# Kernel optimization log

Hardware: AMD Instinct MI355X
Metric: run time of the kernel (lower is better)

The kernel has to match this reference:

```python
import jax, jax.numpy as jnp
import numpy as np

B, S, D, H = 4, 2048, 1024, 16
DH = D // H  # per-head depth = 64


def setup_inputs() -> dict:
    key = jax.random.key(0)
    kq, kk, kv = jax.random.split(key, 3)
    q = jax.random.normal(kq, (B, S, D), dtype=jnp.float32)
    k = jax.random.normal(kk, (B, S, D), dtype=jnp.float32)
    v = jax.random.normal(kv, (B, S, D), dtype=jnp.float32)
    # Standard look-ahead mask: 1.0 where attention is disallowed (j > i).
    mask = (1.0 - jnp.tril(jnp.ones((S, S), dtype=jnp.float32)))[None, None, :, :]
    return {"q": q, "k": k, "v": v, "mask": mask, "training": 0}


def _split_heads(x):
    # [B, S, D] -> [B, H, S, DH]
    b, s, _ = x.shape
    return x.reshape(b, s, H, DH).transpose(0, 2, 1, 3)


def reference(q, k, v, mask, training):
    qh, kh, vh = _split_heads(q), _split_heads(k), _split_heads(v)
    scale = 1.0 / jnp.sqrt(jnp.float32(DH))
    logits = jnp.einsum("bhqd,bhkd->bhqk", qh, kh) * scale  # [B,H,S,S]
    logits = logits + mask * (-1e9)
    weights = jax.nn.softmax(logits, axis=-1)
    attn = jnp.einsum("bhqk,bhkd->bhqd", weights, vh)  # [B,H,S,DH]
    out = attn.transpose(0, 2, 1, 3).reshape(q.shape[0], 1, -1, H * DH)  # [B,1,S,D]
    return out
```

## Files before the change

### kernel.cpp

```cpp
#include <hip/hip_runtime.h>
#include <hip/hip_bf16.h>


constexpr int Ss = 2048, Dd = 1024, Hh = 16, DH = 64, Bb = 4;
constexpr float QSCALE = 0.125f * 1.44269504088896f;
constexpr float MFIX2 = 13.0f;
constexpr float MFIXF = 9.0f;

typedef _Float16 half2_t __attribute__((ext_vector_type(2)));
typedef _Float16 half4_t __attribute__((ext_vector_type(4)));
typedef _Float16 half8_t __attribute__((ext_vector_type(8)));
typedef __attribute__((ext_vector_type(4))) float floatx4;
typedef __attribute__((ext_vector_type(8))) short short8;

union H8 { half8_t v; half2_t h2[4]; };

__device__ __forceinline__ half2_t pk(float a, float b) {
  return __builtin_bit_cast(half2_t, __builtin_amdgcn_cvt_pkrtz(a, b));
}
__device__ __forceinline__ float fexp2(float x) {
#if __has_builtin(__builtin_amdgcn_exp2f)
  return __builtin_amdgcn_exp2f(x);
#else
  return __exp2f(x);
#endif
}
__device__ __forceinline__ unsigned short f2bf(float f) {
  union { float f; unsigned u; } x; x.f = f;
  unsigned r = x.u + 0x7FFFu + ((x.u >> 16) & 1u);
  return (unsigned short)(r >> 16);
}
__device__ __forceinline__ unsigned short f2bf_trunc(float f) {
  union { float f; unsigned u; } x; x.f = f;
  return (unsigned short)(x.u >> 16);
}
__device__ __forceinline__ void async_cp16(const unsigned short* g, unsigned short* l) {
  __builtin_amdgcn_global_load_lds(
      (const __attribute__((address_space(1))) unsigned int*)g,
      (__attribute__((address_space(3))) unsigned int*)l, 16, 0, 0);
}

__global__ __launch_bounds__(256)
void prep_kv(const float* __restrict__ Kg, const float* __restrict__ Vg,
             unsigned short* __restrict__ Kh, unsigned short* __restrict__ Vt) {
  __shared__ float tile[64][65];
  const int s0 = (int)blockIdx.x * 64;
  const int bh = (int)blockIdx.y;
  const int b = bh >> 4, h = bh & 15;
  const int t = threadIdx.x;
  const int sl = t >> 2, qtr = t & 3;

  const size_t inoff = ((size_t)(b * Ss + s0 + sl)) * Dd + h * DH + qtr * 16;
  const float* krow = Kg + inoff;
  const float* vrow = Vg + inoff;
  const int pout = (2 * (sl >> 5) + ((sl & 7) >> 2)) * 16 + ((sl >> 3) & 3) * 4 + (sl & 3);
  unsigned short* kout = Kh + ((size_t)bh * Ss + s0 + pout) * 64 + qtr * 16;

  #pragma unroll
  for (int i = 0; i < 2; ++i) {
    float4 k0 = ((const float4*)krow)[i * 2 + 0];
    float4 k1 = ((const float4*)krow)[i * 2 + 1];
    H8 o;
    o.h2[0] = pk(k0.x, k0.y); o.h2[1] = pk(k0.z, k0.w);
    o.h2[2] = pk(k1.x, k1.y); o.h2[3] = pk(k1.z, k1.w);
    *(half8_t*)(kout + i * 8) = o.v;
  }
  #pragma unroll
  for (int i = 0; i < 4; ++i) {
    float4 v = ((const float4*)vrow)[i];
    tile[sl][qtr * 16 + i * 4 + 0] = v.x;
    tile[sl][qtr * 16 + i * 4 + 1] = v.y;
    tile[sl][qtr * 16 + i * 4 + 2] = v.z;
    tile[sl][qtr * 16 + i * 4 + 3] = v.w;
  }
  __syncthreads();
  const int d = t >> 2, kc = t & 3;
  unsigned short* orow = Vt + ((size_t)bh * DH + d) * Ss + s0 + kc * 16;
  #pragma unroll
  for (int i = 0; i < 2; ++i) {
    H8 o;
    o.h2[0] = pk(tile[kc * 16 + i * 8 + 0][d], tile[kc * 16 + i * 8 + 1][d]);
    o.h2[1] = pk(tile[kc * 16 + i * 8 + 2][d], tile[kc * 16 + i * 8 + 3][d]);
    o.h2[2] = pk(tile[kc * 16 + i * 8 + 4][d], tile[kc * 16 + i * 8 + 5][d]);
    o.h2[3] = pk(tile[kc * 16 + i * 8 + 6][d], tile[kc * 16 + i * 8 + 7][d]);
    *(half8_t*)(orow + i * 8) = o.v;
  }
}

__global__ __launch_bounds__(256, 2)
void mha_fa9(const float* __restrict__ Qg, const unsigned short* __restrict__ Kh,
             const unsigned short* __restrict__ Vt, float* __restrict__ Og) {
  __shared__ __align__(16) unsigned short Kld[2][128 * 64];
  __shared__ __align__(16) unsigned short Vld[2][64 * 128];

  const int tid = threadIdx.x;
  const int wave = tid >> 6, lane = tid & 63;
  const int c = lane & 15, qd = lane >> 4;
  const int bh = (int)blockIdx.x;
  const int b = bh >> 4, h = bh & 15;
  const int slot = (int)blockIdx.y;
  const int t = (slot < 4) ? slot : 11 - slot;
  const int Qt[2] = {2 * t + 1, 2 * t};
  const int nkt = 2 * t + 2;

  const unsigned short* kbase = Kh + (size_t)bh * Ss * 64;
  const unsigned short* vbase = Vt + (size_t)bh * DH * Ss;
  float* obase = Og + (size_t)b * Ss * Dd + h * DH;

  auto stage = [&](int kt, int bufi) {
    const unsigned short* ktile = kbase + kt * 128 * 64;
    #pragma unroll
    for (int it = 0; it < 4; ++it) {
      int p = (it * 4 + wave) * 64 + lane;
      int r = p >> 3, pos = p & 7, j = pos ^ (r & 7);
      async_cp16(ktile + r * 64 + j * 8, &Kld[bufi][(it * 4 + wave) * 512]);
    }
    #pragma unroll
    for (int it = 0; it < 4; ++it) {
      int p = (it * 4 + wave) * 64 + lane;
      int d = p >> 4, c16 = p & 15;
      int j = (c16 & 8) | ((c16 ^ d) & 7);
      async_cp16(vbase + (size_t)d * Ss + kt * 128 + j * 8,
                 &Vld[bufi][(it * 4 + wave) * 512]);
    }
  };

  auto load_frags = [&](const unsigned short* Kl, const unsigned short* Vl, int kb,
                        half8_t (&kf0)[4], half8_t (&kf1)[4], half8_t (&w8)[4][2]) {
    #pragma unroll
    for (int f = 0; f < 4; ++f) {
      int kk = kb * 64 + f * 16 + c;
      kf0[f] = *(const half8_t*)&Kl[kk * 64 + (qd ^ (c & 7)) * 8];
      kf1[f] = *(const half8_t*)&Kl[kk * 64 + ((4 + qd) ^ (c & 7)) * 8];
    }
    #pragma unroll
    for (int f = 0; f < 4; ++f) {
      int rr = f * 16 + c;
      #pragma unroll
      for (int wnd = 0; wnd < 2; ++wnd) {
        int chi = kb * 8 + wnd * 4 + qd;
        int phys = (chi & 8) | ((chi ^ rr) & 7);
        w8[f][wnd] = *(const half8_t*)&Vl[rr * 128 + phys * 8];
      }
    }
  };

  const half8_t ones8 = {(_Float16)1.f, (_Float16)1.f, (_Float16)1.f, (_Float16)1.f,
                         (_Float16)1.f, (_Float16)1.f, (_Float16)1.f, (_Float16)1.f};

  half8_t qf[2][2][2];
  #pragma unroll
  for (int ti = 0; ti < 2; ++ti) {
    #pragma unroll
    for (int mi = 0; mi < 2; ++mi) {
      const float* qr =
          Qg + ((size_t)b * Ss + Qt[ti] * 128 + mi * 64 + wave * 16 + c) * Dd + h * DH;
      #pragma unroll
      for (int ks = 0; ks < 2; ++ks) {
        float4 a0 = ((const float4*)(qr + ks * 32 + qd * 8))[0];
        float4 a1 = ((const float4*)(qr + ks * 32 + qd * 8))[1];
        H8 f;
        f.h2[0] = pk(a0.x * QSCALE, a0.y * QSCALE);
        f.h2[1] = pk(a0.z * QSCALE, a0.w * QSCALE);
        f.h2[2] = pk(a1.x * QSCALE, a1.y * QSCALE);
        f.h2[3] = pk(a1.z * QSCALE, a1.w * QSCALE);
        qf[ti][mi][ks] = f.v;
      }
    }
  }

  floatx4 o_acc[2][2][4];
  floatx4 l_acc[2][2];
  #pragma unroll
  for (int ti = 0; ti < 2; ++ti)
    #pragma unroll
    for (int mi = 0; mi < 2; ++mi) {
      #pragma unroll
      for (int f = 0; f < 4; ++f) o_acc[ti][mi][f] = (floatx4){0.f, 0.f, 0.f, 0.f};
      l_acc[ti][mi] = (floatx4){0.f, 0.f, 0.f, 0.f};
    }

  auto compute_kb = [&](int kb0g, const half8_t (&kf0)[4], const half8_t (&kf1)[4],
                        const half8_t (&w8)[4][2]) {
    #pragma unroll
    for (int ti = 0; ti < 2; ++ti) {
      #pragma unroll
      for (int mi = 0; mi < 2; ++mi) {
        const int qlo = Qt[ti] * 128 + mi * 64 + wave * 16;
        if (kb0g > qlo + 15) continue;

        floatx4 s[4];
        #pragma unroll
        for (int f = 0; f < 4; ++f) s[f] = (floatx4){0.f, 0.f, 0.f, 0.f};
        __builtin_amdgcn_s_setprio(1);
        #pragma unroll
        for (int f = 0; f < 4; ++f) {
          s[f] = __builtin_amdgcn_mfma_f32_16x16x32_f16(kf0[f], qf[ti][mi][0], s[f], 0, 0, 0);
          s[f] = __builtin_amdgcn_mfma_f32_16x16x32_f16(kf1[f], qf[ti][mi][1], s[f], 0, 0, 0);
        }
        __builtin_amdgcn_s_setprio(0);
        if (kb0g + 63 > qlo) {
          #pragma unroll
          for (int f = 0; f < 4; ++f) {
            int keyb = kb0g + ((f >> 1) << 5) + ((f & 1) << 2) + qd * 8;
            #pragma unroll
            for (int r = 0; r < 4; ++r)
              if (keyb + r > qlo + c) s[f][r] = -1e30f;
          }
        }
        half8_t p8[2];
        #pragma unroll
        for (int wnd = 0; wnd < 2; ++wnd) {
          H8 pp;
          pp.h2[0] = pk(fexp2(s[2 * wnd][0] - MFIX2), fexp2(s[2 * wnd][1] - MFIX2));
          pp.h2[1] = pk(fexp2(s[2 * wnd][2] - MFIX2), fexp2(s[2 * wnd][3] - MFIX2));
          pp.h2[2] = pk(fexp2(s[2 * wnd + 1][0] - MFIX2), fexp2(s[2 * wnd + 1][1] - MFIX2));
          pp.h2[3] = pk(fexp2(s[2 * wnd + 1][2] - MFIX2), fexp2(s[2 * wnd + 1][3] - MFIX2));
          p8[wnd] = pp.v;
        }
        __builtin_amdgcn_s_setprio(1);
        #pragma unroll
        for (int fd = 0; fd < 4; ++fd) {
          #pragma unroll
          for (int wnd = 0; wnd < 2; ++wnd)
            o_acc[ti][mi][fd] = __builtin_amdgcn_mfma_f32_16x16x32_f16(
                p8[wnd], w8[fd][wnd], o_acc[ti][mi][fd], 0, 0, 0);
        }
        #pragma unroll
        for (int wnd = 0; wnd < 2; ++wnd)
          l_acc[ti][mi] = __builtin_amdgcn_mfma_f32_16x16x32_f16(p8[wnd], ones8,
                                                                 l_acc[ti][mi], 0, 0, 0);
        __builtin_amdgcn_s_setprio(0);
      }
    }
  };

  asm volatile("s_waitcnt vmcnt(0)" ::: "memory");
  stage(0, 0);
  stage(1, 1);

  for (int kt = 0; kt < nkt; ++kt) {
    const int bufi = kt & 1;
    if (kt + 1 < nkt) {
      asm volatile("s_waitcnt vmcnt(8)" ::: "memory");
    } else {
      asm volatile("s_waitcnt vmcnt(0)" ::: "memory");
    }
    __builtin_amdgcn_s_barrier();

    const unsigned short* Kl = Kld[bufi];
    const unsigned short* Vl = Vld[bufi];

    half8_t kf0a[4], kf1a[4], w8a[4][2];
    load_frags(Kl, Vl, 0, kf0a, kf1a, w8a);
    compute_kb(kt * 128, kf0a, kf1a, w8a);

    half8_t kf0b[4], kf1b[4], w8b[4][2];
    load_frags(Kl, Vl, 1, kf0b, kf1b, w8b);
    asm volatile("s_waitcnt lgkmcnt(0)" ::: "memory");
    __builtin_amdgcn_s_barrier();
    if (kt + 2 < nkt) stage(kt + 2, bufi);

    compute_kb(kt * 128 + 64, kf0b, kf1b, w8b);
  }

  #pragma unroll
  for (int ti = 0; ti < 2; ++ti)
    #pragma unroll
    for (int mi = 0; mi < 2; ++mi)
      #pragma unroll
      for (int r = 0; r < 4; ++r) {
        float inv = 1.f / l_acc[ti][mi][r];
        size_t row = (size_t)(Qt[ti] * 128 + mi * 64 + wave * 16 + qd * 4 + r);
        #pragma unroll
        for (int f = 0; f < 4; ++f)
          obase[row * Dd + f * 16 + c] = o_acc[ti][mi][f][r] * inv;
      }
}

__global__ __launch_bounds__(256, 4)
void mha_fwd(const float* __restrict__ Qg, const float* __restrict__ Kg,
             const float* __restrict__ Vg, float* __restrict__ Og) {
  __shared__ __align__(16) unsigned short Kldf[64 * 72];
  __shared__ __align__(16) unsigned short Vtldf[64 * 72];
  __shared__ __align__(16) unsigned short Pldf[4 * 16 * 72];
  const int tid = threadIdx.x, wave = tid >> 6, lane = tid & 63;
  const int c = lane & 15, qd = lane >> 4;
  const int qt = (Ss / 64 - 1) - (int)blockIdx.x;
  const int b = (int)blockIdx.y >> 4, h = (int)blockIdx.y & 15;
  const float* qbase = Qg + (size_t)b * Ss * Dd + h * DH;
  const float* kbase = Kg + (size_t)b * Ss * Dd + h * DH;
  const float* vbase = Vg + (size_t)b * Ss * Dd + h * DH;
  short8 qfrag[2];
  {
    const float* qr = qbase + (size_t)(qt * 64 + wave * 16 + c) * Dd + qd * 8;
    for (int ks = 0; ks < 2; ++ks) {
      float4 a0 = ((const float4*)(qr + ks * 32))[0];
      float4 a1 = ((const float4*)(qr + ks * 32))[1];
      short8 f;
      f[0] = (short)f2bf(a0.x * 0.125f); f[1] = (short)f2bf(a0.y * 0.125f);
      f[2] = (short)f2bf(a0.z * 0.125f); f[3] = (short)f2bf(a0.w * 0.125f);
      f[4] = (short)f2bf(a1.x * 0.125f); f[5] = (short)f2bf(a1.y * 0.125f);
      f[6] = (short)f2bf(a1.z * 0.125f); f[7] = (short)f2bf(a1.w * 0.125f);
      qfrag[ks] = f;
    }
  }
  floatx4 o_acc[4];
  for (int f = 0; f < 4; ++f) o_acc[f] = (floatx4){0.f, 0.f, 0.f, 0.f};
  float l_lane[4] = {0.f, 0.f, 0.f, 0.f};
  const int row_g = qt * 64 + wave * 16;
  const int pbase = wave * 16 * 72;
  for (int kt = 0; kt <= qt; ++kt) {
    __syncthreads();
    {
      const int r = tid >> 2, quarter = tid & 3;
      const float* krow = kbase + (size_t)(kt * 64 + r) * Dd + quarter * 16;
      const float* vrow = vbase + (size_t)(kt * 64 + r) * Dd + quarter * 16;
      for (int i = 0; i < 4; ++i) {
        float4 kv = ((const float4*)krow)[i];
        int col = quarter * 16 + i * 4;
        ushort4 kk;
        kk.x = f2bf(kv.x); kk.y = f2bf(kv.y); kk.z = f2bf(kv.z); kk.w = f2bf(kv.w);
        *(ushort4*)&Kldf[r * 72 + col] = kk;
        float4 vv = ((const float4*)vrow)[i];
        Vtldf[(col + 0) * 72 + r] = f2bf(vv.x);
        Vtldf[(col + 1) * 72 + r] = f2bf(vv.y);
        Vtldf[(col + 2) * 72 + r] = f2bf(vv.z);
        Vtldf[(col + 3) * 72 + r] = f2bf(vv.w);
      }
    }
    __syncthreads();
    floatx4 s_acc[4];
    for (int f = 0; f < 4; ++f) s_acc[f] = (floatx4){0.f, 0.f, 0.f, 0.f};
    for (int f = 0; f < 4; ++f)
      for (int ks = 0; ks < 2; ++ks) {
        short8 kf = *(const short8*)&Kldf[(f * 16 + c) * 72 + ks * 32 + qd * 8];
        s_acc[f] = __builtin_amdgcn_mfma_f32_16x16x32_bf16(qfrag[ks], kf, s_acc[f], 0, 0, 0);
      }
    if (kt == qt)
      for (int f = 0; f < 4; ++f) {
        int key = kt * 64 + f * 16 + c;
        for (int r = 0; r < 4; ++r)
          if (key > row_g + qd * 4 + r) s_acc[f][r] = -1e30f;
      }
    for (int f = 0; f < 4; ++f)
      for (int r = 0; r < 4; ++r) {
        float p = __expf(s_acc[f][r] - MFIXF);
        l_lane[r] += p;
        Pldf[pbase + (qd * 4 + r) * 72 + f * 16 + c] = f2bf_trunc(p);
      }
    short8 pfrag[2];
    pfrag[0] = *(const short8*)&Pldf[pbase + c * 72 + qd * 8];
    pfrag[1] = *(const short8*)&Pldf[pbase + c * 72 + 32 + qd * 8];
    for (int f = 0; f < 4; ++f)
      for (int ks = 0; ks < 2; ++ks) {
        short8 vf = *(const short8*)&Vtldf[(f * 16 + c) * 72 + ks * 32 + qd * 8];
        o_acc[f] = __builtin_amdgcn_mfma_f32_16x16x32_bf16(pfrag[ks], vf, o_acc[f], 0, 0, 0);
      }
  }
  float* obase = Og + (size_t)b * Ss * Dd + h * DH;
  for (int r = 0; r < 4; ++r) {
    float lv = l_lane[r];
    lv += __shfl_xor(lv, 1); lv += __shfl_xor(lv, 2);
    lv += __shfl_xor(lv, 4); lv += __shfl_xor(lv, 8);
    float inv_l = 1.f / lv;
    size_t rowoff = (size_t)(row_g + qd * 4 + r) * Dd;
    for (int f = 0; f < 4; ++f)
      obase[rowoff + f * 16 + c] = o_acc[f][r] * inv_l;
  }
}

extern "C" void kernel_launch(void* const* d_in, const int* in_sizes, int n_in,
                              void* d_out, int out_size, void* d_ws, size_t ws_size,
                              hipStream_t stream) {
  const float* q = (const float*)d_in[0];
  const float* k = (const float*)d_in[1];
  const float* v = (const float*)d_in[2];
  float* out = (float*)d_out;

  const size_t elems = (size_t)Bb * Hh * Ss * DH;
  if (ws_size >= 2 * elems * 2) {
    unsigned short* kh = (unsigned short*)d_ws;
    unsigned short* vt = kh + elems;
    prep_kv<<<dim3(Ss / 64, Bb * Hh), 256, 0, stream>>>(k, v, kh, vt);
    mha_fa9<<<dim3(Bb * Hh, 8), 256, 0, stream>>>(q, kh, vt, out);
  } else {
    mha_fwd<<<dim3(Ss / 64, Bb * Hh), 256, 0, stream>>>(q, k, v, out);
  }
}
```

Baseline: 201.9 us.

## Split attention block across 8 waves, one 64-row half per wave group

The fused attention kernel now launches 512 threads per block instead of 256. The mi (64-row half) loop becomes a wave index, so each wave handles half the query rows and keeps half the accumulators and Q fragments. K/V staging is spread over 8 waves with fewer copies each, and the vmcnt wait threshold is adjusted to match. The aim is more waves in flight to hide latency and a lower per-wave register footprint, at the cost of every wave reading the full K/V fragments from LDS (more LDS traffic per FLOP) and a heavier barrier.

```diff
diff --git a/kernel.cpp b/kernel.cpp
--- a/kernel.cpp
+++ b/kernel.cpp
@@ -87,14 +87,15 @@
   }
 }
 
-__global__ __launch_bounds__(256, 2)
-void mha_fa9(const float* __restrict__ Qg, const unsigned short* __restrict__ Kh,
-             const unsigned short* __restrict__ Vt, float* __restrict__ Og) {
+__global__ __launch_bounds__(512, 4)
+void mha_fa10(const float* __restrict__ Qg, const unsigned short* __restrict__ Kh,
+              const unsigned short* __restrict__ Vt, float* __restrict__ Og) {
   __shared__ __align__(16) unsigned short Kld[2][128 * 64];
   __shared__ __align__(16) unsigned short Vld[2][64 * 128];
 
   const int tid = threadIdx.x;
   const int wave = tid >> 6, lane = tid & 63;
+  const int wv = wave & 3, mi = wave >> 2;
   const int c = lane & 15, qd = lane >> 4;
   const int bh = (int)blockIdx.x;
   const int b = bh >> 4, h = bh & 15;
@@ -110,18 +111,20 @@
   auto stage = [&](int kt, int bufi) {
     const unsigned short* ktile = kbase + kt * 128 * 64;
     #pragma unroll
-    for (int it = 0; it < 4; ++it) {
-      int p = (it * 4 + wave) * 64 + lane;
+    for (int it = 0; it < 2; ++it) {
+      int idx = it * 8 + wave;
+      int p = idx * 64 + lane;
       int r = p >> 3, pos = p & 7, j = pos ^ (r & 7);
-      async_cp16(ktile + r * 64 + j * 8, &Kld[bufi][(it * 4 + wave) * 512]);
-    }
-    #pragma unroll
-    for (int it = 0; it < 4; ++it) {
-      int p = (it * 4 + wave) * 64 + lane;
+      async_cp16(ktile + r * 64 + j * 8, &Kld[bufi][idx * 512]);
+    }
+    #pragma unroll
+    for (int it = 0; it < 2; ++it) {
+      int idx = it * 8 + wave;
+      int p = idx * 64 + lane;
       int d = p >> 4, c16 = p & 15;
       int j = (c16 & 8) | ((c16 ^ d) & 7);
       async_cp16(vbase + (size_t)d * Ss + kt * 128 + j * 8,
-                 &Vld[bufi][(it * 4 + wave) * 512]);
+                 &Vld[bufi][idx * 512]);
     }
   };
 
@@ -148,90 +151,82 @@
   const half8_t ones8 = {(_Float16)1.f, (_Float16)1.f, (_Float16)1.f, (_Float16)1.f,
                          (_Float16)1.f, (_Float16)1.f, (_Float16)1.f, (_Float16)1.f};
 
-  half8_t qf[2][2][2];
+  half8_t qf[2][2];
   #pragma unroll
   for (int ti = 0; ti < 2; ++ti) {
-    #pragma unroll
-    for (int mi = 0; mi < 2; ++mi) {
-      const float* qr =
-          Qg + ((size_t)b * Ss + Qt[ti] * 128 + mi * 64 + wave * 16 + c) * Dd + h * DH;
-      #pragma unroll
-      for (int ks = 0; ks < 2; ++ks) {
-        float4 a0 = ((const float4*)(qr + ks * 32 + qd * 8))[0];
-        float4 a1 = ((const float4*)(qr + ks * 32 + qd * 8))[1];
-        H8 f;
-        f.h2[0] = pk(a0.x * QSCALE, a0.y * QSCALE);
-        f.h2[1] = pk(a0.z * QSCALE, a0.w * QSCALE);
-        f.h2[2] = pk(a1.x * QSCALE, a1.y * QSCALE);
-        f.h2[3] = pk(a1.z * QSCALE, a1.w * QSCALE);
-        qf[ti][mi][ks] = f.v;
-      }
-    }
-  }
-
-  floatx4 o_acc[2][2][4];
-  floatx4 l_acc[2][2];
-  #pragma unroll
-  for (int ti = 0; ti < 2; ++ti)
-    #pragma unroll
-    for (int mi = 0; mi < 2; ++mi) {
-      #pragma unroll
-      for (int f = 0; f < 4; ++f) o_acc[ti][mi][f] = (floatx4){0.f, 0.f, 0.f, 0.f};
-      l_acc[ti][mi] = (floatx4){0.f, 0.f, 0.f, 0.f};
-    }
+    const float* qr =
+        Qg + ((size_t)b * Ss + Qt[ti] * 128 + mi * 64 + wv * 16 + c) * Dd + h * DH;
+    #pragma unroll
+    for (int ks = 0; ks < 2; ++ks) {
+      float4 a0 = ((const float4*)(qr + ks * 32 + qd * 8))[0];
+      float4 a1 = ((const float4*)(qr + ks * 32 + qd * 8))[1];
+      H8 f;
+      f.h2[0] = pk(a0.x * QSCALE, a0.y * QSCALE);
+      f.h2[1] = pk(a0.z * QSCALE, a0.w * QSCALE);
+      f.h2[2] = pk(a1.x * QSCALE, a1.y * QSCALE);
+      f.h2[3] = pk(a1.z * QSCALE, a1.w * QSCALE);
+      qf[ti][ks] = f.v;
+    }
+  }
+
+  floatx4 o_acc[2][4];
+  floatx4 l_acc[2];
+  #pragma unroll
+  for (int ti = 0; ti < 2; ++ti) {
+    #pragma unroll
+    for (int f = 0; f < 4; ++f) o_acc[ti][f] = (floatx4){0.f, 0.f, 0.f, 0.f};
+    l_acc[ti] = (floatx4){0.f, 0.f, 0.f, 0.f};
+  }
 
   auto compute_kb = [&](int kb0g, const half8_t (&kf0)[4], const half8_t (&kf1)[4],
                         const half8_t (&w8)[4][2]) {
     #pragma unroll
     for (int ti = 0; ti < 2; ++ti) {
-      #pragma unroll
-      for (int mi = 0; mi < 2; ++mi) {
-        const int qlo = Qt[ti] * 128 + mi * 64 + wave * 16;
-        if (kb0g > qlo + 15) continue;
-
-        floatx4 s[4];
-        #pragma unroll
-        for (int f = 0; f < 4; ++f) s[f] = (floatx4){0.f, 0.f, 0.f, 0.f};
-        __builtin_amdgcn_s_setprio(1);
+      const int qlo = Qt[ti] * 128 + mi * 64 + wv * 16;
+      if (kb0g > qlo + 15) continue;
+
+      floatx4 s[4];
+      #pragma unroll
+      for (int f = 0; f < 4; ++f) s[f] = (floatx4){0.f, 0.f, 0.f, 0.f};
+      __builtin_amdgcn_s_setprio(1);
+      #pragma unroll
+      for (int f = 0; f < 4; ++f) {
+        s[f] = __builtin_amdgcn_mfma_f32_16x16x32_f16(kf0[f], qf[ti][0], s[f], 0, 0, 0);
+        s[f] = __builtin_amdgcn_mfma_f32_16x16x32_f16(kf1[f], qf[ti][1], s[f], 0, 0, 0);
+      }
+      __builtin_amdgcn_s_setprio(0);
+      if (kb0g + 63 > qlo) {
         #pragma unroll
         for (int f = 0; f < 4; ++f) {
-          s[f] = __builtin_amdgcn_mfma_f32_16x16x32_f16(kf0[f], qf[ti][mi][0], s[f], 0, 0, 0);
-          s[f] = __builtin_amdgcn_mfma_f32_16x16x32_f16(kf1[f], qf[ti][mi][1], s[f], 0, 0, 0);
+          int keyb = kb0g + ((f >> 1) << 5) + ((f & 1) << 2) + qd * 8;
+          #pragma unroll
+          for (int r = 0; r < 4; ++r)
+            if (keyb + r > qlo + c) s[f][r] = -1e30f;
         }
-        __builtin_amdgcn_s_setprio(0);
-        if (kb0g + 63 > qlo) {
-          #pragma unroll
-          for (int f = 0; f < 4; ++f) {
-            int keyb = kb0g + ((f >> 1) << 5) + ((f & 1) << 2) + qd * 8;
-            #pragma unroll
-            for (int r = 0; r < 4; ++r)
-              if (keyb + r > qlo + c) s[f][r] = -1e30f;
-          }
-        }
-        half8_t p8[2];
-        #pragma unroll
-        for (int wnd = 0; wnd < 2; ++wnd) {
-          H8 pp;
-          pp.h2[0] = pk(fexp2(s[2 * wnd][0] - MFIX2), fexp2(s[2 * wnd][1] - MFIX2));
-          pp.h2[1] = pk(fexp2(s[2 * wnd][2] - MFIX2), fexp2(s[2 * wnd][3] - MFIX2));
-          pp.h2[2] = pk(fexp2(s[2 * wnd + 1][0] - MFIX2), fexp2(s[2 * wnd + 1][1] - MFIX2));
-          pp.h2[3] = pk(fexp2(s[2 * wnd + 1][2] - MFIX2), fexp2(s[2 * wnd + 1][3] - MFIX2));
-          p8[wnd] = pp.v;
-        }
-        __builtin_amdgcn_s_setprio(1);
-        #pragma unroll
-        for (int fd = 0; fd < 4; ++fd) {
-          #pragma unroll
-          for (int wnd = 0; wnd < 2; ++wnd)
-            o_acc[ti][mi][fd] = __builtin_amdgcn_mfma_f32_16x16x32_f16(
-                p8[wnd], w8[fd][wnd], o_acc[ti][mi][fd], 0, 0, 0);
-        }
+      }
+      half8_t p8[2];
+      #pragma unroll
+      for (int wnd = 0; wnd < 2; ++wnd) {
+        H8 pp;
+        pp.h2[0] = pk(fexp2(s[2 * wnd][0] - MFIX2), fexp2(s[2 * wnd][1] - MFIX2));
+        pp.h2[1] = pk(fexp2(s[2 * wnd][2] - MFIX2), fexp2(s[2 * wnd][3] - MFIX2));
+        pp.h2[2] = pk(fexp2(s[2 * wnd + 1][0] - MFIX2), fexp2(s[2 * wnd + 1][1] - MFIX2));
+        pp.h2[3] = pk(fexp2(s[2 * wnd + 1][2] - MFIX2), fexp2(s[2 * wnd + 1][3] - MFIX2));
+        p8[wnd] = pp.v;
+      }
+      __builtin_amdgcn_s_setprio(1);
+      #pragma unroll
+      for (int fd = 0; fd < 4; ++fd) {
         #pragma unroll
         for (int wnd = 0; wnd < 2; ++wnd)
-          l_acc[ti][mi] = __builtin_amdgcn_mfma_f32_16x16x32_f16(p8[wnd], ones8,
-                                                                 l_acc[ti][mi], 0, 0, 0);
-        __builtin_amdgcn_s_setprio(0);
-      }
+          o_acc[ti][fd] = __builtin_amdgcn_mfma_f32_16x16x32_f16(
+              p8[wnd], w8[fd][wnd], o_acc[ti][fd], 0, 0, 0);
+      }
+      #pragma unroll
+      for (int wnd = 0; wnd < 2; ++wnd)
+        l_acc[ti] = __builtin_amdgcn_mfma_f32_16x16x32_f16(p8[wnd], ones8,
+                                                           l_acc[ti], 0, 0, 0);
+      __builtin_amdgcn_s_setprio(0);
     }
   };
 
@@ -242,7 +237,7 @@
   for (int kt = 0; kt < nkt; ++kt) {
     const int bufi = kt & 1;
     if (kt + 1 < nkt) {
-      asm volatile("s_waitcnt vmcnt(8)" ::: "memory");
+      asm volatile("s_waitcnt vmcnt(4)" ::: "memory");
     } else {
       asm volatile("s_waitcnt vmcnt(0)" ::: "memory");
     }
@@ -267,15 +262,13 @@
   #pragma unroll
   for (int ti = 0; ti < 2; ++ti)
     #pragma unroll
-    for (int mi = 0; mi < 2; ++mi)
-      #pragma unroll
-      for (int r = 0; r < 4; ++r) {
-        float inv = 1.f / l_acc[ti][mi][r];
-        size_t row = (size_t)(Qt[ti] * 128 + mi * 64 + wave * 16 + qd * 4 + r);
-        #pragma unroll
-        for (int f = 0; f < 4; ++f)
-          obase[row * Dd + f * 16 + c] = o_acc[ti][mi][f][r] * inv;
-      }
+    for (int r = 0; r < 4; ++r) {
+      float inv = 1.f / l_acc[ti][r];
+      size_t row = (size_t)(Qt[ti] * 128 + mi * 64 + wv * 16 + qd * 4 + r);
+      #pragma unroll
+      for (int f = 0; f < 4; ++f)
+        obase[row * Dd + f * 16 + c] = o_acc[ti][f][r] * inv;
+    }
 }
 
 __global__ __launch_bounds__(256, 4)
@@ -383,7 +376,7 @@
     unsigned short* kh = (unsigned short*)d_ws;
     unsigned short* vt = kh + elems;
     prep_kv<<<dim3(Ss / 64, Bb * Hh), 256, 0, stream>>>(k, v, kh, vt);
-    mha_fa9<<<dim3(Bb * Hh, 8), 256, 0, stream>>>(q, kh, vt, out);
+    mha_fa10<<<dim3(Bb * Hh, 8), 512, 0, stream>>>(q, kh, vt, out);
   } else {
     mha_fwd<<<dim3(Ss / 64, Bb * Hh), 256, 0, stream>>>(q, k, v, out);
   }
```

Measured after the change: 315.2 us. +56.1%, slower.
